# Kernel tuning notes

Measured on AMD Instinct MI355X. Metric: run time of the kernel, lower is better.

## Reference

```python
import jax, jax.numpy as jnp
import numpy as np

B, S, HID = 4, 2048, 1024
NH = 16
HD = HID // NH  # 64


def setup_inputs() -> dict:
    key = jax.random.key(0)
    k1, k2, k3 = jax.random.split(key, 3)
    x = jax.random.normal(k1, (B, S, HID), dtype=jnp.float32)
    # causal sparse mask: True = attend
    mask = jnp.tril(jnp.ones((S, S), dtype=bool))
    w_qkv = jax.random.normal(k2, (HID, 3 * HID), dtype=jnp.float32) * 0.02
    b_qkv = jnp.zeros((3 * HID,), dtype=jnp.float32)
    w_out = jax.random.normal(k3, (HID, HID), dtype=jnp.float32) * 0.02
    b_out = jnp.zeros((HID,), dtype=jnp.float32)
    return {"x": x, "mask": mask, "w_qkv": w_qkv, "b_qkv": b_qkv,
            "w_out": w_out, "b_out": b_out}


def reference(x, mask, w_qkv, b_qkv, w_out, b_out):
    bsz, seq_len, hid = x.shape
    # QKV projection -> [B, S, H, 3*D] -> [B, H, S, 3*D]
    qkv = (x @ w_qkv + b_qkv).reshape(bsz, seq_len, NH, 3 * HD).transpose(0, 2, 1, 3)
    q, k, v = jnp.split(qkv, 3, axis=-1)  # each [B, H, S, D]
    scale = 1.0 / jnp.sqrt(jnp.asarray(HD, dtype=x.dtype))
    scores = jnp.einsum('bhqd,bhkd->bhqk', q, k) * scale
    scores = jnp.where(mask[None, None, :, :], scores, jnp.asarray(-jnp.inf, dtype=scores.dtype))
    probs = jax.nn.softmax(scores, axis=-1)
    context = jnp.einsum('bhqk,bhkd->bhqd', probs, v)  # [B, H, S, D]
    context = context.transpose(0, 2, 1, 3).reshape(bsz, seq_len, hid)
    return context @ w_out + b_out
```

## Files before the change

kernel.cpp:

```cpp
#include <hip/hip_runtime.h>
#include <stdint.h>

#define S_LEN 2048
#define NHEAD 16
#define HDIM  64
#define HIDDEN 1024
#define BATCH 4

typedef float f32x4 __attribute__((ext_vector_type(4)));
typedef __bf16 bf16x8 __attribute__((ext_vector_type(8)));
typedef unsigned short u16;

union U4B8 { uint4 u; bf16x8 b; };

__device__ __forceinline__ bf16x8 as_b8(uint4 u){ U4B8 x; x.u = u; return x.b; }

__device__ __forceinline__ f32x4 mfma16(uint4 a, uint4 b, f32x4 c){
  return __builtin_amdgcn_mfma_f32_16x16x32_bf16(as_b8(a), as_b8(b), c, 0, 0, 0);
}

__device__ __forceinline__ u16 f2bf(float f){
  __bf16 h = (__bf16)f;
  return __builtin_bit_cast(u16, h);
}

__device__ __forceinline__ float exp2fast(float x){
  return __builtin_exp2f(x);
}

__device__ __forceinline__ void gload16(const void* g, void* l){
  __builtin_amdgcn_global_load_lds(
      (const __attribute__((address_space(1))) unsigned int*)g,
      (__attribute__((address_space(3))) unsigned int*)l, 16, 0, 0);
}

#define QSCALE 0.18033688f
#define DEFER_THR 11.5f

__global__ __launch_bounds__(256) void k_cvt(const float* __restrict__ in,
                                             u16* __restrict__ out, int n4){
  int i = blockIdx.x * 256 + threadIdx.x;
  int stride = gridDim.x * 256;
  for (; i < n4; i += stride){
    float4 v = ((const float4*)in)[i];
    unsigned lo = (unsigned)f2bf(v.x) | ((unsigned)f2bf(v.y) << 16);
    unsigned hi = (unsigned)f2bf(v.z) | ((unsigned)f2bf(v.w) << 16);
    ((uint2*)out)[i] = make_uint2(lo, hi);
  }
}

__global__ __launch_bounds__(256) void k_transpose(const float* __restrict__ in,
                                                   u16* __restrict__ out,
                                                   int K, int N){
  __shared__ float t[32][33];
  int tx = threadIdx.x & 31, ty = threadIdx.x >> 5;
  int n0 = blockIdx.x * 32, k0 = blockIdx.y * 32;
  #pragma unroll
  for (int i = 0; i < 4; ++i)
    t[ty + i*8][tx] = in[(size_t)(k0 + ty + i*8) * N + n0 + tx];
  __syncthreads();
  #pragma unroll
  for (int i = 0; i < 4; ++i)
    out[(size_t)(n0 + ty + i*8) * K + k0 + tx] = f2bf(t[tx][ty + i*8]);
}

__device__ __forceinline__ void stage_gemm(
    const u16* __restrict__ A, const u16* __restrict__ Bt,
    u16* As, u16* Bs, int row0, int col0, int K, int k0, int wave, int lane)
{
  #pragma unroll
  for (int p = 0; p < 2; ++p){
    int chunk = wave * 128 + p * 64 + lane;
    int r = chunk >> 2, cseg = chunk & 3;
    int sseg = cseg ^ (r & 3);
    const u16* ga = A  + (size_t)(row0 + r) * K + k0 + sseg * 8;
    gload16(ga, As + (size_t)(wave * 128 + p * 64) * 8);
    const u16* gb = Bt + (size_t)(col0 + r) * K + k0 + sseg * 8;
    gload16(gb, Bs + (size_t)(wave * 128 + p * 64) * 8);
  }
}

template<int MODE>
__global__ __launch_bounds__(256) void k_gemm(
    const u16* __restrict__ A, const u16* __restrict__ Bt,
    const float* __restrict__ bias,
    u16* __restrict__ oq, u16* __restrict__ ok, u16* __restrict__ ov,
    float* __restrict__ of, int M, int N, int K, int nx)
{
  __shared__ u16 As[3][128 * 32];
  __shared__ u16 Bs[3][128 * 32];
  const int tid  = threadIdx.x;
  const int wave = tid >> 6, lane = tid & 63;
  const int l4 = lane >> 4, lm = lane & 15;
  const int wr = wave >> 1, wc = wave & 1;

  const int bid = blockIdx.x;
  const int nwg = gridDim.x;
  const int ny8 = nwg / (8 * nx);
  const int xcd = bid & 7, t = bid >> 3;
  const int by = xcd * ny8 + t / nx;
  const int bx = t % nx;
  const int row0 = by * 128;
  const int col0 = bx * 128;

  const f32x4 fzero = {0.f, 0.f, 0.f, 0.f};
  f32x4 acc[4][4];
  #pragma unroll
  for (int m = 0; m < 4; ++m)
    #pragma unroll
    for (int n = 0; n < 4; ++n) acc[m][n] = fzero;

  const int nks = K >> 5;
  stage_gemm(A, Bt, &As[0][0], &Bs[0][0], row0, col0, K, 0, wave, lane);
  stage_gemm(A, Bt, &As[1][0], &Bs[1][0], row0, col0, K, 32, wave, lane);

  int cur = 0;
  #pragma unroll 1
  for (int ks = 0; ks < nks; ++ks){
    if (ks + 2 < nks){
      int nxt = cur + 2; if (nxt >= 3) nxt -= 3;
      stage_gemm(A, Bt, &As[nxt][0], &Bs[nxt][0],
                 row0, col0, K, (ks + 2) << 5, wave, lane);
      asm volatile("s_waitcnt vmcnt(8)" ::: "memory");
    } else if (ks + 1 < nks){
      asm volatile("s_waitcnt vmcnt(4)" ::: "memory");
    } else {
      asm volatile("s_waitcnt vmcnt(0)" ::: "memory");
    }
    __builtin_amdgcn_s_barrier();
    asm volatile("" ::: "memory");

    uint4 af[4], bf[4];
    #pragma unroll
    for (int m = 0; m < 4; ++m){
      int rr = wr * 64 + m * 16 + lm;
      af[m] = *(const uint4*)&As[cur][rr * 32 + (l4 ^ (rr & 3)) * 8];
    }
    #pragma unroll
    for (int n = 0; n < 4; ++n){
      int rr = wc * 64 + n * 16 + lm;
      bf[n] = *(const uint4*)&Bs[cur][rr * 32 + (l4 ^ (rr & 3)) * 8];
    }
    __builtin_amdgcn_s_setprio(1);
    #pragma unroll
    for (int m = 0; m < 4; ++m)
      #pragma unroll
      for (int n = 0; n < 4; ++n)
        acc[m][n] = mfma16(af[m], bf[n], acc[m][n]);
    __builtin_amdgcn_s_setprio(0);

    asm volatile("" ::: "memory");
    __builtin_amdgcn_s_barrier();
    asm volatile("" ::: "memory");

    cur = cur + 1; if (cur >= 3) cur -= 3;
  }

  #pragma unroll
  for (int m = 0; m < 4; ++m){
    #pragma unroll
    for (int n = 0; n < 4; ++n){
      int c = col0 + wc * 64 + n * 16 + lm;
      float bv = bias[c];
      #pragma unroll
      for (int r = 0; r < 4; ++r){
        int row = row0 + wr * 64 + m * 16 + l4 * 4 + r;
        float val = acc[m][n][r] + bv;
        if (MODE == 0){
          int h = c / 192, e = c % 192;
          int which = e >> 6, d = e & 63;
          int b = row >> 11, s = row & 2047;
          int bh = b * 16 + h;
          if (which == 2){
            ov[((size_t)bh * HDIM + d) * S_LEN + s] = f2bf(val);
          } else {
            if (which == 0) val *= QSCALE;
            size_t idx = ((size_t)bh * S_LEN + s) * HDIM + d;
            u16* dst = (which == 0) ? oq : ok;
            dst[idx] = f2bf(val);
          }
        } else {
          of[(size_t)row * N + c] = val;
        }
      }
    }
  }
}

__device__ __forceinline__ void stage_tile8(
    const u16* __restrict__ kB, const u16* __restrict__ vB,
    u16* ldsK, u16* ldsV, int kbase, int wave, int lane)
{
  int ch  = wave * 64 + lane;
  int row = ch >> 3;
  int cc  = (ch & 7) << 4;
  int sc  = cc ^ ((row & 7) << 4);
  gload16(kB + (size_t)(kbase + row) * HDIM + (sc >> 1), ldsK + (size_t)wave * 512);
  gload16(vB + (size_t)row * S_LEN + kbase + (sc >> 1), ldsV + (size_t)wave * 512);
}

__global__ __launch_bounds__(512) void k_attn(
    const u16* __restrict__ q, const u16* __restrict__ kk,
    const u16* __restrict__ vt, u16* __restrict__ ctx)
{
  __shared__ u16 KV[2][2][64 * 64];
  __shared__ u16 Ps[8][16][72];

  const int bid = blockIdx.x;
  const int bh = bid & 63;
  const int pr = bid >> 6;
  const int wave = threadIdx.x >> 6, lane = threadIdx.x & 63;
  const int l4 = lane >> 4, lm = lane & 15;
  const size_t base = (size_t)bh * (S_LEN * HDIM);
  const u16* kB = kk + base;
  const u16* vB = vt + base;
  const int b = bh >> 4, h = bh & 15;
  const f32x4 fz = {0.f, 0.f, 0.f, 0.f};

  #pragma unroll 1
  for (int half = 0; half < 2; ++half){
    const int st = half ? (15 - pr) : pr;
    const int q0 = st * 128 + wave * 16;

    uint4 qf0, qf1;
    {
      const u16* qr = q + base + (size_t)(q0 + lm) * HDIM + l4 * 8;
      qf0 = *(const uint4*)qr;
      qf1 = *(const uint4*)(qr + 32);
    }

    float mr = -1e30f, lsp = 0.f;
    f32x4 acc[4];
    #pragma unroll
    for (int tt = 0; tt < 4; ++tt) acc[tt] = fz;

    const int nkt = 2 * st + 2;

    stage_tile8(kB, vB, &KV[0][0][0], &KV[0][1][0], 0, wave, lane);

    #pragma unroll 1
    for (int kt = 0; kt < nkt; ++kt){
      const int cur = kt & 1;
      const int kbase = kt << 6;
      if (kt + 1 < nkt){
        stage_tile8(kB, vB, &KV[cur ^ 1][0][0], &KV[cur ^ 1][1][0],
                    (kt + 1) << 6, wave, lane);
        asm volatile("s_waitcnt vmcnt(2)" ::: "memory");
      } else {
        asm volatile("s_waitcnt vmcnt(0)" ::: "memory");
      }
      __builtin_amdgcn_s_barrier();
      asm volatile("" ::: "memory");

      if (kbase < q0 + 16){
        const u16* ldsK = &KV[cur][0][0];
        const u16* ldsV = &KV[cur][1][0];

        f32x4 sv[4];
        __builtin_amdgcn_s_setprio(1);
        #pragma unroll
        for (int g = 0; g < 4; ++g){
          int rk = g * 16 + lm;
          int xa = (l4 * 16) ^ ((rk & 7) << 4);
          int xb = (64 + l4 * 16) ^ ((rk & 7) << 4);
          const u16* krow = ldsK + rk * 64;
          uint4 kf0 = *(const uint4*)(krow + (xa >> 1));
          uint4 kf1 = *(const uint4*)(krow + (xb >> 1));
          sv[g] = mfma16(kf0, qf0, fz);
          sv[g] = mfma16(kf1, qf1, sv[g]);
        }
        __builtin_amdgcn_s_setprio(0);

        if (kbase + 63 > q0){
          #pragma unroll
          for (int g = 0; g < 4; ++g)
            #pragma unroll
            for (int r = 0; r < 4; ++r){
              int kg = kbase + g * 16 + l4 * 4 + r;
              int qg = q0 + lm;
              if (kg > qg) sv[g][r] = -1e30f;
            }
        }

        float pml = sv[0][0];
        #pragma unroll
        for (int g = 0; g < 4; ++g)
          #pragma unroll
          for (int r = 0; r < 4; ++r) pml = fmaxf(pml, sv[g][r]);

        if (__any(pml > mr + DEFER_THR)){
          float pm = fmaxf(pml, __shfl_xor(pml, 16));
          pm = fmaxf(pm, __shfl_xor(pm, 32));
          float mn = fmaxf(mr, pm);
          float corr = exp2fast(mr - mn);
          mr = mn;
          lsp *= corr;
          float cf[4];
          #pragma unroll
          for (int r = 0; r < 4; ++r) cf[r] = __shfl(corr, l4 * 4 + r);
          #pragma unroll
          for (int tt = 0; tt < 4; ++tt)
            #pragma unroll
            for (int r = 0; r < 4; ++r) acc[tt][r] *= cf[r];
        }

        float s_ = 0.f;
        #pragma unroll
        for (int g = 0; g < 4; ++g){
          float p0 = exp2fast(sv[g][0] - mr);
          float p1 = exp2fast(sv[g][1] - mr);
          float p2 = exp2fast(sv[g][2] - mr);
          float p3 = exp2fast(sv[g][3] - mr);
          s_ += (p0 + p1) + (p2 + p3);
          uint2 w;
          w.x = (unsigned)f2bf(p0) | ((unsigned)f2bf(p1) << 16);
          w.y = (unsigned)f2bf(p2) | ((unsigned)f2bf(p3) << 16);
          *(uint2*)&Ps[wave][lm][g * 16 + l4 * 4] = w;
        }
        lsp += s_;

        __builtin_amdgcn_wave_barrier();
        uint4 pa0 = *(const uint4*)&Ps[wave][lm][l4 * 8];
        uint4 pa1 = *(const uint4*)&Ps[wave][lm][32 + l4 * 8];

        __builtin_amdgcn_s_setprio(1);
        #pragma unroll
        for (int tt = 0; tt < 4; ++tt){
          int rv = tt * 16 + lm;
          int xa = (l4 * 16) ^ ((rv & 7) << 4);
          int xb = (64 + l4 * 16) ^ ((rv & 7) << 4);
          const u16* vrow = ldsV + rv * 64;
          uint4 v0 = *(const uint4*)(vrow + (xa >> 1));
          uint4 v1 = *(const uint4*)(vrow + (xb >> 1));
          acc[tt] = mfma16(pa0, v0, acc[tt]);
          acc[tt] = mfma16(pa1, v1, acc[tt]);
        }
        __builtin_amdgcn_s_setprio(0);
      }

      asm volatile("" ::: "memory");
      __builtin_amdgcn_s_barrier();
      asm volatile("" ::: "memory");
    }

    lsp += __shfl_xor(lsp, 16);
    lsp += __shfl_xor(lsp, 32);
    float inv_ = 1.0f / lsp;
    float ivr[4];
    #pragma unroll
    for (int r = 0; r < 4; ++r) ivr[r] = __shfl(inv_, l4 * 4 + r);
    #pragma unroll
    for (int tt = 0; tt < 4; ++tt)
      #pragma unroll
      for (int r = 0; r < 4; ++r){
        int srow = q0 + l4 * 4 + r;
        float val = acc[tt][r] * ivr[r];
        ctx[((size_t)b * S_LEN + srow) * HIDDEN + h * HDIM + tt * 16 + lm] = f2bf(val);
      }
  }
}

extern "C" void kernel_launch(void* const* d_in, const int* in_sizes, int n_in,
                              void* d_out, int out_size, void* d_ws, size_t ws_size,
                              hipStream_t stream)
{
  const float* x     = (const float*)d_in[0];
  const float* w_qkv = (const float*)d_in[2];
  const float* b_qkv = (const float*)d_in[3];
  const float* w_out = (const float*)d_in[4];
  const float* b_out = (const float*)d_in[5];

  char* ws = (char*)d_ws;
  u16* xbf   = (u16*)(ws);
  u16* wqkvT = (u16*)(ws + 16777216);
  u16* woutT = (u16*)(ws + 23068672);
  u16* qb    = (u16*)(ws + 25165824);
  u16* kb    = (u16*)(ws + 41943040);
  u16* vb    = (u16*)(ws + 58720256);

  k_cvt<<<2048, 256, 0, stream>>>(x, xbf, (BATCH * S_LEN * HIDDEN) / 4);
  k_transpose<<<dim3(96, 32), 256, 0, stream>>>(w_qkv, wqkvT, HIDDEN, 3 * HIDDEN);
  k_transpose<<<dim3(32, 32), 256, 0, stream>>>(w_out, woutT, HIDDEN, HIDDEN);
  k_gemm<0><<<24 * 64, 256, 0, stream>>>(xbf, wqkvT, b_qkv,
                                         qb, kb, vb, nullptr,
                                         BATCH * S_LEN, 3 * HIDDEN, HIDDEN, 24);
  k_attn<<<512, 512, 0, stream>>>(qb, kb, vb, xbf);
  k_gemm<1><<<8 * 64, 256, 0, stream>>>(xbf, woutT, b_out,
                                        nullptr, nullptr, nullptr,
                                        (float*)d_out, BATCH * S_LEN, HIDDEN, HIDDEN, 8);
}
```

Measured before the change: 196.2 us.

## Use 256x256-tile 8-wave ping-pong GEMM for QKV projection

```diff
diff --git a/kernel.cpp b/kernel.cpp
--- a/kernel.cpp
+++ b/kernel.cpp
@@ -36,6 +36,9 @@
 
 #define QSCALE 0.18033688f
 #define DEFER_THR 11.5f
+
+#define FENCE asm volatile("" ::: "memory")
+#define PH_BAR do{ FENCE; __builtin_amdgcn_s_barrier(); FENCE; }while(0)
 
 __global__ __launch_bounds__(256) void k_cvt(const float* __restrict__ in,
                                              u16* __restrict__ out, int n4){
@@ -64,6 +67,163 @@
     out[(size_t)(n0 + ty + i*8) * K + k0 + tx] = f2bf(t[tx][ty + i*8]);
 }
 
+__global__ __launch_bounds__(512, 2) void k_gemm8(
+    const u16* __restrict__ A, const u16* __restrict__ Bt,
+    const float* __restrict__ bias,
+    u16* __restrict__ oq, u16* __restrict__ ok, u16* __restrict__ ov,
+    int M, int N, int K, int nx)
+{
+  __shared__ u16 As[4][256 * 32];
+  __shared__ u16 Bs[4][256 * 32];
+  const int tid  = threadIdx.x;
+  const int wave = tid >> 6, lane = tid & 63;
+  const int l4 = lane >> 4, lm = lane & 15;
+  const int wr = wave >> 2, wc = wave & 3;
+
+  const int bid = blockIdx.x, nwg = gridDim.x;
+  const int ny8 = nwg / (8 * nx);
+  const int xcd = bid & 7, tq = bid >> 3;
+  const int by = xcd * ny8 + tq / nx;
+  const int bx = tq % nx;
+  const int row0 = by * 256, col0 = bx * 256;
+
+  int aOff[8], bOff[4];
+  #pragma unroll
+  for (int m = 0; m < 8; ++m){
+    int r = wr * 128 + m * 16 + lm;
+    aOff[m] = r * 32 + ((l4 ^ (lm & 3)) << 3);
+  }
+  #pragma unroll
+  for (int n = 0; n < 4; ++n){
+    int r = wc * 64 + n * 16 + lm;
+    bOff[n] = r * 32 + ((l4 ^ (lm & 3)) << 3);
+  }
+
+  auto stageA = [&](int kt, int slot){
+    int k0 = kt << 5;
+    #pragma unroll
+    for (int p = 0; p < 2; ++p){
+      int ch = p * 512 + wave * 64 + lane;
+      int r = ch >> 2, ss = (ch & 3) ^ (r & 3);
+      gload16(A + (size_t)(row0 + r) * K + k0 + ss * 8,
+              &As[slot][(p * 512 + wave * 64) * 8]);
+    }
+  };
+  auto stageB = [&](int kt, int slot){
+    int k0 = kt << 5;
+    #pragma unroll
+    for (int p = 0; p < 2; ++p){
+      int ch = p * 512 + wave * 64 + lane;
+      int r = ch >> 2, ss = (ch & 3) ^ (r & 3);
+      gload16(Bt + (size_t)(col0 + r) * K + k0 + ss * 8,
+              &Bs[slot][(p * 512 + wave * 64) * 8]);
+    }
+  };
+
+  f32x4 acc[8][4];
+  const f32x4 fz = {0.f, 0.f, 0.f, 0.f};
+  #pragma unroll
+  for (int m = 0; m < 8; ++m)
+    #pragma unroll
+    for (int n = 0; n < 4; ++n) acc[m][n] = fz;
+
+  const int nT = K >> 5;
+  const int nI = nT >> 1;
+
+  stageA(0, 0); stageB(0, 0);
+  stageA(1, 1); stageB(1, 1);
+  stageA(2, 2); stageB(2, 2);
+  asm volatile("s_waitcnt vmcnt(8)" ::: "memory");
+  PH_BAR;
+
+  uint4 alo[4], ahi[4], bE[4], bO[4];
+  #pragma unroll
+  for (int m = 0; m < 4; ++m) alo[m] = *(const uint4*)&As[0][aOff[m]];
+  #pragma unroll
+  for (int n = 0; n < 4; ++n) bE[n]  = *(const uint4*)&Bs[0][bOff[n]];
+
+#define MFMA_BLK(AF, BF, MB) \
+  __builtin_amdgcn_s_setprio(1); \
+  _Pragma("unroll") \
+  for (int m_ = 0; m_ < 4; ++m_) \
+    _Pragma("unroll") \
+    for (int n_ = 0; n_ < 4; ++n_) \
+      acc[(MB) + m_][n_] = mfma16(AF[m_], BF[n_], acc[(MB) + m_][n_]); \
+  __builtin_amdgcn_s_setprio(0);
+
+  #pragma unroll 1
+  for (int i = 0; i < nI; ++i){
+    const int t0 = 2 * i;
+    const int sl0 = t0 & 3, sl1 = (t0 + 1) & 3, sl2 = (t0 + 2) & 3;
+    const int sg1 = (t0 + 3) & 3, sg2 = (t0 + 4) & 3;
+    const int tg1 = (t0 + 3 < nT) ? t0 + 3 : nT - 1;
+    const int tg2 = (t0 + 4 < nT) ? t0 + 4 : nT - 1;
+
+    stageA(tg1, sg1);
+    #pragma unroll
+    for (int m = 0; m < 4; ++m) ahi[m] = *(const uint4*)&As[sl0][aOff[4 + m]];
+    asm volatile("s_waitcnt vmcnt(6)" ::: "memory");
+    __builtin_amdgcn_sched_barrier(0);
+    MFMA_BLK(alo, bE, 0);
+    PH_BAR;
+
+    stageB(tg1, sg1);
+    #pragma unroll
+    for (int m = 0; m < 4; ++m) alo[m] = *(const uint4*)&As[sl1][aOff[m]];
+    #pragma unroll
+    for (int n = 0; n < 4; ++n) bO[n]  = *(const uint4*)&Bs[sl1][bOff[n]];
+    __builtin_amdgcn_sched_barrier(0);
+    MFMA_BLK(ahi, bE, 4);
+    PH_BAR;
+
+    stageA(tg2, sg2);
+    #pragma unroll
+    for (int m = 0; m < 4; ++m) ahi[m] = *(const uint4*)&As[sl1][aOff[4 + m]];
+    asm volatile("s_waitcnt vmcnt(6)" ::: "memory");
+    __builtin_amdgcn_sched_barrier(0);
+    MFMA_BLK(alo, bO, 0);
+    PH_BAR;
+
+    stageB(tg2, sg2);
+    if (i + 1 < nI){
+      #pragma unroll
+      for (int m = 0; m < 4; ++m) alo[m] = *(const uint4*)&As[sl2][aOff[m]];
+      #pragma unroll
+      for (int n = 0; n < 4; ++n) bE[n]  = *(const uint4*)&Bs[sl2][bOff[n]];
+    }
+    __builtin_amdgcn_sched_barrier(0);
+    MFMA_BLK(ahi, bO, 4);
+    PH_BAR;
+  }
+#undef MFMA_BLK
+
+  #pragma unroll
+  for (int m = 0; m < 8; ++m){
+    #pragma unroll
+    for (int n = 0; n < 4; ++n){
+      int c = col0 + wc * 64 + n * 16 + lm;
+      float bv = bias[c];
+      #pragma unroll
+      for (int r = 0; r < 4; ++r){
+        int row = row0 + wr * 128 + m * 16 + l4 * 4 + r;
+        float val = acc[m][n][r] + bv;
+        int h = c / 192, e = c % 192;
+        int which = e >> 6, d = e & 63;
+        int b = row >> 11, s = row & 2047;
+        int bh = b * 16 + h;
+        if (which == 2){
+          ov[((size_t)bh * HDIM + d) * S_LEN + s] = f2bf(val);
+        } else {
+          if (which == 0) val *= QSCALE;
+          size_t idx = ((size_t)bh * S_LEN + s) * HDIM + d;
+          u16* dst = (which == 0) ? oq : ok;
+          dst[idx] = f2bf(val);
+        }
+      }
+    }
+  }
+}
+
 __device__ __forceinline__ void stage_gemm(
     const u16* __restrict__ A, const u16* __restrict__ Bt,
     u16* As, u16* Bs, int row0, int col0, int K, int k0, int wave, int lane)
@@ -80,11 +240,9 @@
   }
 }
 
-template<int MODE>
-__global__ __launch_bounds__(256) void k_gemm(
+__global__ __launch_bounds__(256) void k_gemm_out(
     const u16* __restrict__ A, const u16* __restrict__ Bt,
     const float* __restrict__ bias,
-    u16* __restrict__ oq, u16* __restrict__ ok, u16* __restrict__ ov,
     float* __restrict__ of, int M, int N, int K, int nx)
 {
   __shared__ u16 As[3][128 * 32];
@@ -127,8 +285,7 @@
     } else {
       asm volatile("s_waitcnt vmcnt(0)" ::: "memory");
     }
-    __builtin_amdgcn_s_barrier();
-    asm volatile("" ::: "memory");
+    PH_BAR;
 
     uint4 af[4], bf[4];
     #pragma unroll
@@ -149,9 +306,7 @@
         acc[m][n] = mfma16(af[m], bf[n], acc[m][n]);
     __builtin_amdgcn_s_setprio(0);
 
-    asm volatile("" ::: "memory");
-    __builtin_amdgcn_s_barrier();
-    asm volatile("" ::: "memory");
+    PH_BAR;
 
     cur = cur + 1; if (cur >= 3) cur -= 3;
   }
@@ -165,23 +320,7 @@
       #pragma unroll
       for (int r = 0; r < 4; ++r){
         int row = row0 + wr * 64 + m * 16 + l4 * 4 + r;
-        float val = acc[m][n][r] + bv;
-        if (MODE == 0){
-          int h = c / 192, e = c % 192;
-          int which = e >> 6, d = e & 63;
-          int b = row >> 11, s = row & 2047;
-          int bh = b * 16 + h;
-          if (which == 2){
-            ov[((size_t)bh * HDIM + d) * S_LEN + s] = f2bf(val);
-          } else {
-            if (which == 0) val *= QSCALE;
-            size_t idx = ((size_t)bh * S_LEN + s) * HDIM + d;
-            u16* dst = (which == 0) ? oq : ok;
-            dst[idx] = f2bf(val);
-          }
-        } else {
-          of[(size_t)row * N + c] = val;
-        }
+        of[(size_t)row * N + c] = acc[m][n][r] + bv;
       }
     }
   }
@@ -249,8 +388,7 @@
       } else {
         asm volatile("s_waitcnt vmcnt(0)" ::: "memory");
       }
-      __builtin_amdgcn_s_barrier();
-      asm volatile("" ::: "memory");
+      PH_BAR;
 
       if (kbase < q0 + 16){
         const u16* ldsK = &KV[cur][0][0];
@@ -338,9 +476,7 @@
         __builtin_amdgcn_s_setprio(0);
       }
 
-      asm volatile("" ::: "memory");
-      __builtin_amdgcn_s_barrier();
-      asm volatile("" ::: "memory");
+      PH_BAR;
     }
 
     lsp += __shfl_xor(lsp, 16);
@@ -381,11 +517,9 @@
   k_cvt<<<2048, 256, 0, stream>>>(x, xbf, (BATCH * S_LEN * HIDDEN) / 4);
   k_transpose<<<dim3(96, 32), 256, 0, stream>>>(w_qkv, wqkvT, HIDDEN, 3 * HIDDEN);
   k_transpose<<<dim3(32, 32), 256, 0, stream>>>(w_out, woutT, HIDDEN, HIDDEN);
-  k_gemm<0><<<24 * 64, 256, 0, stream>>>(xbf, wqkvT, b_qkv,
-                                         qb, kb, vb, nullptr,
-                                         BATCH * S_LEN, 3 * HIDDEN, HIDDEN, 24);
+  k_gemm8<<<384, 512, 0, stream>>>(xbf, wqkvT, b_qkv, qb, kb, vb,
+                                   BATCH * S_LEN, 3 * HIDDEN, HIDDEN, 12);
   k_attn<<<512, 512, 0, stream>>>(qb, kb, vb, xbf);
-  k_gemm<1><<<8 * 64, 256, 0, stream>>>(xbf, woutT, b_out,
-                                        nullptr, nullptr, nullptr,
-                                        (float*)d_out, BATCH * S_LEN, HIDDEN, HIDDEN, 8);
-}
+  k_gemm_out<<<8 * 64, 256, 0, stream>>>(xbf, woutT, b_out,
+                                         (float*)d_out, BATCH * S_LEN, HIDDEN, HIDDEN, 8);
+}
```

New measurement: 213.1 us. 1.09x slower.
